# Kernel tuning notes

Measured on AMD Instinct MI355X. Metric: run time of the kernel, lower is better.

The kernel has to match this reference:

```python
import jax, jax.numpy as jnp
import numpy as np

B, S, D, R, N = 4, 2048, 1024, 256, 16

def setup_inputs() -> dict:
    key = jax.random.key(0)
    k1, k2, k3, k4, k5 = jax.random.split(key, 5)
    return {
        "x": jax.random.normal(k1, (B, S, D), dtype=jnp.float32),
        "feature_know": jax.random.normal(k2, (N, D, R), dtype=jnp.float32) * 0.02,
        "restore_know": jax.random.normal(k3, (N, R, D), dtype=jnp.float32) * 0.02,
        "feature_know_w": jax.random.uniform(k4, (B, S, N), dtype=jnp.float32),
        "restore_know_w": jax.random.uniform(k5, (B, S, N), dtype=jnp.float32),
    }

def reference(x, feature_know, restore_know, feature_know_w, restore_know_w):
    # Feature stage: weighted mixture over N knowledge neurons, D -> R.
    # Same math as einsum('bsd,ndr->bsnr') then einsum('bsnr,bsn->bsr'),
    # fused so the [B,S,N,R] intermediate is reduced over N on the fly.
    h = jnp.einsum('bsd,ndr,bsn->bsr', x, feature_know, feature_know_w)
    # Restore stage: R -> D, again a weighted mixture over N neurons.
    out = jnp.einsum('bsr,nrd,bsn->bsd', h, restore_know, restore_know_w)
    # Dropout is evaluated deterministically (eval mode): identity.
    return out
```

## Files before the change

### kernel.cpp

```cpp
#include <hip/hip_runtime.h>

typedef unsigned short u16;
typedef unsigned int u32;
typedef __attribute__((ext_vector_type(4))) float f32x4;
typedef __attribute__((ext_vector_type(8))) short bf16x8;
typedef __attribute__((ext_vector_type(4))) unsigned short u16x4;

#define MFMA(a, b, c) __builtin_amdgcn_mfma_f32_16x16x32_bf16((a), (b), (c), 0, 0, 0)

static constexpr int M_TOK = 8192;

__device__ __forceinline__ u16 f2bf(float f) {
  u32 u = __float_as_uint(f);
  return (u16)((u + 0x7FFFu + ((u >> 16) & 1u)) >> 16);
}
__device__ __forceinline__ float bf2f(u16 b) {
  u32 u = ((u32)b) << 16;
  return __uint_as_float(u);
}
__device__ __forceinline__ void gload16(const u16* g, u16* l) {
  __builtin_amdgcn_global_load_lds(
      (const __attribute__((address_space(1))) u32*)(const void*)g,
      (__attribute__((address_space(3))) u32*)(void*)l, 16, 0, 0);
}

#define PH_BAR()                                     \
  do {                                               \
    __builtin_amdgcn_sched_barrier(0);               \
    __builtin_amdgcn_s_barrier();                    \
    asm volatile("s_waitcnt lgkmcnt(0)" ::: "memory"); \
    __builtin_amdgcn_sched_barrier(0);               \
  } while (0)
#define PH_END()                       \
  do {                                 \
    __builtin_amdgcn_sched_barrier(0); \
    __builtin_amdgcn_s_barrier();      \
  } while (0)

__global__ void cast_x_kernel(const float* __restrict__ in, u16* __restrict__ out, int total4) {
  for (int i = blockIdx.x * blockDim.x + threadIdx.x; i < total4; i += gridDim.x * blockDim.x) {
    float4 v = ((const float4*)in)[i];
    u16x4 o;
    o[0] = f2bf(v.x); o[1] = f2bf(v.y); o[2] = f2bf(v.z); o[3] = f2bf(v.w);
    ((u16x4*)out)[i] = o;
  }
}

__global__ void tcast_kernel(const float* __restrict__ in, u16* __restrict__ out, int P, int Q) {
  __shared__ float tile[32][33];
  const int z = blockIdx.z;
  const int q0 = blockIdx.x * 32, p0 = blockIdx.y * 32;
  const float* src = in + (size_t)z * P * Q;
  u16* dst = out + (size_t)z * P * Q;
  const int tx = threadIdx.x & 31, ty = threadIdx.x >> 5;
#pragma unroll
  for (int k = 0; k < 4; ++k)
    tile[ty + k * 8][tx] = src[(size_t)(p0 + ty + k * 8) * Q + q0 + tx];
  __syncthreads();
#pragma unroll
  for (int k = 0; k < 4; ++k)
    dst[(size_t)(q0 + ty + k * 8) * P + p0 + tx] = f2bf(tile[tx][ty + k * 8]);
}

__global__ void combine_h(const u16* __restrict__ T, const float* __restrict__ Wf,
                          u16* __restrict__ h) {
  const int m = blockIdx.x * 4 + (threadIdx.x >> 6);
  const int lane = threadIdx.x & 63;
  const u16* rowp = T + (size_t)m * 4096;
  float h0 = 0.f, h1 = 0.f, h2 = 0.f, h3 = 0.f;
#pragma unroll
  for (int n = 0; n < 16; ++n) {
    u16x4 v = *(const u16x4*)&rowp[n * 256 + lane * 4];
    const float wf = Wf[(size_t)m * 16 + n];
    h0 += wf * bf2f(v[0]); h1 += wf * bf2f(v[1]);
    h2 += wf * bf2f(v[2]); h3 += wf * bf2f(v[3]);
  }
  u16x4 o;
  o[0] = f2bf(h0); o[1] = f2bf(h1); o[2] = f2bf(h2); o[3] = f2bf(h3);
  *(u16x4*)&h[(size_t)m * 256 + lane * 4] = o;
}

template <int NT>
__global__ __launch_bounds__(512, 2) void gemm256(
    const u16* __restrict__ A, const u16* __restrict__ Bm, void* __restrict__ OutV,
    const int N, const int K) {
  constexpr int NITER = NT / 2;
  __shared__ u16 ldsA[2][2][8192];
  __shared__ u16 ldsB[2][2][8192];

  const int tid = threadIdx.x;
  const int lane = tid & 63;
  const int wid = tid >> 6;
  const int wr = wid >> 2, wc = wid & 3;

  {
  }
  const int L = blockIdx.y * gridDim.x + blockIdx.x;
  const int ordered = (L & 7) * 64 + (L >> 3);
  const int cid = ordered >> 5, win = ordered & 31;
  const int bx = (cid & 3) * 4 + (win & 3);
  const int by = (cid >> 2) * 8 + (win >> 2);
  const int m0 = by * 256, bn0 = bx * 256;

  const int arow = lane & 15;
  const int acol = (lane >> 4) * 16;
  const int sw = (arow & 7) << 4;
  const int lo0 = arow * 128 + (acol ^ sw);
  const int lo1 = arow * 128 + ((64 + acol) ^ sw);

  const u16* Abase = A + (size_t)m0 * K;
  const u16* Bbase = Bm + (size_t)bn0 * K;

  f32x4 acc[8][4];
#pragma unroll
  for (int i = 0; i < 8; ++i)
#pragma unroll
    for (int j = 0; j < 4; ++j) acc[i][j] = (f32x4){0.f, 0.f, 0.f, 0.f};

  auto STAGE = [&](int b, int isB, int hf, int kt) {
    const u16* G = isB ? Bbase : Abase;
    u16* L2p = isB ? &ldsB[b][hf][0] : &ldsA[b][hf][0];
#pragma unroll
    for (int j = 0; j < 2; ++j) {
      const int q = j * 8192 + tid * 16;
      const int grow = q >> 7;
      const int gcol = ((q & 127) ^ (((q >> 7) & 7) << 4)) >> 1;
      gload16(G + (size_t)(hf * 128 + grow) * K + kt * 64 + gcol,
              L2p + ((j * 8192 + wid * 1024) >> 1));
    }
  };
  auto LOAD_AV = [&](bf16x8 (&v)[4][2], int b, int mh) {
    const char* p = (const char*)&ldsA[b][0][0] + (wr * 128 + mh * 64) * 128;
#pragma unroll
    for (int mi = 0; mi < 4; ++mi) {
      v[mi][0] = *(const bf16x8*)(p + mi * 2048 + lo0);
      v[mi][1] = *(const bf16x8*)(p + mi * 2048 + lo1);
    }
  };
  auto LOAD_BV = [&](bf16x8 (&v)[2][2], int b, int nq) {
#pragma unroll
    for (int nj = 0; nj < 2; ++nj) {
      const int rb = wc * 64 + (nq * 2 + nj) * 16;
      const char* p = (const char*)&ldsB[b][0][0] + rb * 128;
      v[nj][0] = *(const bf16x8*)(p + lo0);
      v[nj][1] = *(const bf16x8*)(p + lo1);
    }
  };

#define QUAD(AV, BV, MH, NQ)                                                   \
  do {                                                                         \
    _Pragma("unroll") for (int mi = 0; mi < 4; ++mi) {                         \
      _Pragma("unroll") for (int nj = 0; nj < 2; ++nj) {                       \
        acc[(MH)*4 + mi][(NQ)*2 + nj] =                                        \
            MFMA(AV[mi][0], BV[nj][0], acc[(MH)*4 + mi][(NQ)*2 + nj]);         \
        acc[(MH)*4 + mi][(NQ)*2 + nj] =                                        \
            MFMA(AV[mi][1], BV[nj][1], acc[(MH)*4 + mi][(NQ)*2 + nj]);         \
      }                                                                        \
    }                                                                          \
  } while (0)

  bf16x8 av[4][2], avh[4][2], bv0[2][2], bv1[2][2];

  STAGE(0, 0, 0, 0); STAGE(0, 0, 1, 0); STAGE(0, 1, 0, 0); STAGE(0, 1, 1, 0);
  STAGE(1, 1, 0, 1); STAGE(1, 0, 0, 1);
  asm volatile("s_waitcnt vmcnt(4)" ::: "memory");
  __builtin_amdgcn_sched_barrier(0);
  __builtin_amdgcn_s_barrier();

#pragma unroll 1
  for (int i = 0; i < NITER; ++i) {
    const int ta = 2 * i, tb = ta + 1;
    const bool st = (i + 1 < NITER);
    LOAD_AV(av, 0, 0); LOAD_BV(bv0, 0, 0); LOAD_BV(bv1, 0, 1);
    STAGE(1, 0, 1, tb); STAGE(1, 1, 1, tb);
    PH_BAR();
    __builtin_amdgcn_s_setprio(1);
    QUAD(av, bv0, 0, 0); QUAD(av, bv1, 0, 1);
    __builtin_amdgcn_s_setprio(0);
    PH_END();
    LOAD_AV(avh, 0, 1);
    if (st) { STAGE(0, 1, 0, ta + 2); STAGE(0, 0, 0, ta + 2); }
    PH_BAR();
    __builtin_amdgcn_s_setprio(1);
    QUAD(avh, bv0, 1, 0); QUAD(avh, bv1, 1, 1);
    __builtin_amdgcn_s_setprio(0);
    if (st) asm volatile("s_waitcnt vmcnt(4)" ::: "memory");
    else    asm volatile("s_waitcnt vmcnt(0)" ::: "memory");
    PH_END();
    LOAD_AV(av, 1, 0); LOAD_BV(bv0, 1, 0); LOAD_BV(bv1, 1, 1);
    if (st) { STAGE(0, 0, 1, ta + 2); STAGE(0, 1, 1, ta + 2); }
    PH_BAR();
    __builtin_amdgcn_s_setprio(1);
    QUAD(av, bv0, 0, 0); QUAD(av, bv1, 0, 1);
    __builtin_amdgcn_s_setprio(0);
    PH_END();
    LOAD_AV(avh, 1, 1);
    if (st) { STAGE(1, 1, 0, tb + 2); STAGE(1, 0, 0, tb + 2); }
    PH_BAR();
    __builtin_amdgcn_s_setprio(1);
    QUAD(avh, bv0, 1, 0); QUAD(avh, bv1, 1, 1);
    __builtin_amdgcn_s_setprio(0);
    if (st) asm volatile("s_waitcnt vmcnt(4)" ::: "memory");
    PH_END();
  }

#pragma unroll
  for (int MI = 0; MI < 8; ++MI) {
    const int row = m0 + wr * 128 + MI * 16 + (lane >> 4) * 4;
#pragma unroll
    for (int NJ = 0; NJ < 4; ++NJ) {
      const int col = bn0 + wc * 64 + NJ * 16 + (lane & 15);
      u16* p = (u16*)OutV + (size_t)row * N + col;
#pragma unroll
      for (int j = 0; j < 4; ++j) p[(size_t)j * N] = f2bf(acc[MI][NJ][j]);
    }
  }
}
#undef QUAD

__global__ __launch_bounds__(512, 2) void gemm_fold(
    const u16* __restrict__ A,
    const u16* __restrict__ Bn,
    const float* __restrict__ W,
    float* __restrict__ Out) {
  __shared__ u16 ldsB[8][8192];
  __shared__ u16 Wlds[16][264];

  const int tid = threadIdx.x;
  const int lane = tid & 63;
  const int wid = tid >> 6;
  const int kh = wid >> 2;
  const int wrM = (wid >> 1) & 1;
  const int wcN = wid & 1;

  const int L = blockIdx.y * gridDim.x + blockIdx.x;
  const int ordered = (L & 7) * 64 + (L >> 3);
  const int cid = ordered >> 5, win = ordered & 31;
  const int bx = (cid & 3) * 2 + (win & 1);
  const int by = (cid >> 2) * 16 + (win >> 1);
  const int m0 = by * 128, d0 = bx * 128;

  const int arow = lane & 15;
  const int acol = (lane >> 4) * 16;
  const int sw = (arow & 7) << 4;
  const int lo0 = arow * 128 + (acol ^ sw);
  const int lo1 = arow * 128 + ((64 + acol) ^ sw);

  for (int i = tid; i < 128 * 16; i += 512) {
    const int row = i >> 4, n = i & 15;
    Wlds[n][row] = f2bf(W[(size_t)(m0 + row) * 16 + n]);
  }

  auto ASTAGE = [&](int kt) {
    const u16* G = A + (size_t)m0 * 256;
    u16* Lp = &ldsB[kt][0];
#pragma unroll
    for (int j = 0; j < 2; ++j) {
      const int q = j * 8192 + tid * 16;
      const int grow = q >> 7;
      const int gcol = ((q & 127) ^ (((q >> 7) & 7) << 4)) >> 1;
      gload16(G + (size_t)grow * 256 + kt * 64 + gcol, Lp + ((j * 8192 + wid * 1024) >> 1));
    }
  };
  ASTAGE(0); ASTAGE(1); ASTAGE(2); ASTAGE(3);
  __syncthreads();
  bf16x8 avk[4][4];
#pragma unroll
  for (int c2 = 0; c2 < 2; ++c2) {
#pragma unroll
    for (int mi = 0; mi < 4; ++mi) {
      const char* p = (const char*)&ldsB[kh * 2 + c2][0] + (wrM * 64 + mi * 16) * 128;
      avk[c2 * 2 + 0][mi] = *(const bf16x8*)(p + lo0);
      avk[c2 * 2 + 1][mi] = *(const bf16x8*)(p + lo1);
    }
  }
  __syncthreads();

  auto BSTAGE = [&](int ss) {
    const int n = ss >> 1, h = ss & 1, p = ss & 3;
    const u16* G = Bn + ((size_t)n * 1024 + d0) * 256;
#pragma unroll
    for (int t = 0; t < 2; ++t) {
      u16* Lp = &ldsB[2 * p + t][0];
      const int kt = h + 2 * t;
#pragma unroll
      for (int j = 0; j < 2; ++j) {
        const int q = j * 8192 + tid * 16;
        const int grow = q >> 7;
        const int gcol = ((q & 127) ^ (((q >> 7) & 7) << 4)) >> 1;
        gload16(G + (size_t)grow * 256 + kt * 64 + gcol, Lp + ((j * 8192 + wid * 1024) >> 1));
      }
    }
  };

  f32x4 acc_t[4][4], acc_g[4][4];
#pragma unroll
  for (int mi = 0; mi < 4; ++mi)
#pragma unroll
    for (int nj = 0; nj < 4; ++nj) {
      acc_t[mi][nj] = (f32x4){0.f, 0.f, 0.f, 0.f};
      acc_g[mi][nj] = (f32x4){0.f, 0.f, 0.f, 0.f};
    }
  bf16x8 bv[4][2];

  BSTAGE(0); BSTAGE(1); BSTAGE(2);
  asm volatile("s_waitcnt vmcnt(8)" ::: "memory");
  __builtin_amdgcn_sched_barrier(0);
  __builtin_amdgcn_s_barrier();

  auto SSTEP = [&](int ss, int h, bool do_stage, int vmsel) {
    const int p = ss & 3;
    const char* pB = (const char*)&ldsB[2 * p + kh][0];
#pragma unroll
    for (int nj = 0; nj < 4; ++nj) {
      const char* q = pB + (wcN * 64 + nj * 16) * 128;
      bv[nj][0] = *(const bf16x8*)(q + lo0);
      bv[nj][1] = *(const bf16x8*)(q + lo1);
    }
    if (do_stage) BSTAGE(ss + 3);
    PH_BAR();
    __builtin_amdgcn_s_setprio(1);
#pragma unroll
    for (int mi = 0; mi < 4; ++mi)
#pragma unroll
      for (int nj = 0; nj < 4; ++nj) {
        acc_g[mi][nj] = MFMA(avk[2 * h + 0][mi], bv[nj][0], acc_g[mi][nj]);
        acc_g[mi][nj] = MFMA(avk[2 * h + 1][mi], bv[nj][1], acc_g[mi][nj]);
      }
    __builtin_amdgcn_s_setprio(0);
    if (vmsel == 8)      asm volatile("s_waitcnt vmcnt(8)" ::: "memory");
    else if (vmsel == 4) asm volatile("s_waitcnt vmcnt(4)" ::: "memory");
    else if (vmsel == 0) asm volatile("s_waitcnt vmcnt(0)" ::: "memory");
    PH_END();
  };
  auto FOLD = [&](int n) {
#pragma unroll
    for (int mi = 0; mi < 4; ++mi) {
      const int rbase = wrM * 64 + mi * 16 + (lane >> 4) * 4;
      u16x4 wq = *(const u16x4*)&Wlds[n][rbase];
      const float w0 = bf2f(wq[0]), w1 = bf2f(wq[1]), w2 = bf2f(wq[2]), w3 = bf2f(wq[3]);
#pragma unroll
      for (int nj = 0; nj < 4; ++nj) {
        acc_t[mi][nj][0] += w0 * acc_g[mi][nj][0];
        acc_t[mi][nj][1] += w1 * acc_g[mi][nj][1];
        acc_t[mi][nj][2] += w2 * acc_g[mi][nj][2];
        acc_t[mi][nj][3] += w3 * acc_g[mi][nj][3];
        acc_g[mi][nj] = (f32x4){0.f, 0.f, 0.f, 0.f};
      }
    }
  };

#pragma unroll 1
  for (int nn = 0; nn < 14; ++nn) {
    SSTEP(nn * 2 + 0, 0, true, 8);
    SSTEP(nn * 2 + 1, 1, true, 8);
    FOLD(nn);
  }
  SSTEP(28, 0, true, 8);
  SSTEP(29, 1, false, 4);
  FOLD(14);
  SSTEP(30, 0, false, 0);
  SSTEP(31, 1, false, -1);
  FOLD(15);

  __syncthreads();
  float* red = (float*)&ldsB[0][0];
  const int reg = (wrM * 2 + wcN) * 4096;
  if (kh == 1) {
#pragma unroll
    for (int mi = 0; mi < 4; ++mi)
#pragma unroll
      for (int j = 0; j < 4; ++j) {
        const int r = mi * 16 + (lane >> 4) * 4 + j;
#pragma unroll
        for (int nj = 0; nj < 4; ++nj)
          red[reg + r * 64 + nj * 16 + (lane & 15)] = acc_t[mi][nj][j];
      }
  }
  __syncthreads();
  if (kh == 0) {
#pragma unroll
    for (int mi = 0; mi < 4; ++mi) {
      const int rr = mi * 16 + (lane >> 4) * 4;
#pragma unroll
      for (int j = 0; j < 4; ++j) {
        float* orow = Out + (size_t)(m0 + wrM * 64 + rr + j) * 1024 + d0 + wcN * 64 + (lane & 15);
#pragma unroll
        for (int nj = 0; nj < 4; ++nj)
          orow[nj * 16] = acc_t[mi][nj][j] + red[reg + (rr + j) * 64 + nj * 16 + (lane & 15)];
      }
    }
  }
}

extern "C" void kernel_launch(void* const* d_in, const int* in_sizes, int n_in,
                              void* d_out, int out_size, void* d_ws, size_t ws_size,
                              hipStream_t stream) {
  const float* x  = (const float*)d_in[0];
  const float* F  = (const float*)d_in[1];
  const float* Rk = (const float*)d_in[2];
  const float* Wf = (const float*)d_in[3];
  const float* Wr = (const float*)d_in[4];
  float* out = (float*)d_out;

  char* ws = (char*)d_ws;
  u16* X16 = (u16*)(ws);
  u16* B1  = (u16*)(ws + (16u << 20));
  u16* Rt  = (u16*)(ws + (24u << 20));
  u16* T   = (u16*)(ws + (32u << 20));
  u16* h16 = (u16*)(ws);

  cast_x_kernel<<<2048, 256, 0, stream>>>(x, X16, (M_TOK * 1024) / 4);
  tcast_kernel<<<dim3(8, 32, 16), 256, 0, stream>>>(F, B1, 1024, 256);
  tcast_kernel<<<dim3(32, 8, 16), 256, 0, stream>>>(Rk, Rt, 256, 1024);

  gemm256<16><<<dim3(16, 32, 1), 512, 0, stream>>>(X16, B1, T, 4096, 1024);
  combine_h<<<2048, 256, 0, stream>>>(T, Wf, h16);
  gemm_fold<<<dim3(8, 64, 1), 512, 0, stream>>>(h16, Rt, Wr, out);
}
```

Before: 171.0 us.

## Stage GEMM epilogues through swizzled LDS for coalesced vector stores; reorder MFMA k-loop

Both GEMM kernels now write their output tiles into a swizzled LDS buffer first and then store them to global memory with 16-byte vector writes, replacing the scattered 2- and 4-byte per-lane stores. The fold kernel's cross-half reduction also goes through this LDS tile before the coalesced write. The MFMA loops are reordered so the k-slice index is outermost, which spaces out dependent accumulator updates. The cost is extra LDS traffic and barriers in the epilogue, plus reuse of the operand LDS buffers for output staging.

```diff
diff --git a/kernel.cpp b/kernel.cpp
--- a/kernel.cpp
+++ b/kernel.cpp
@@ -85,16 +85,13 @@
     const u16* __restrict__ A, const u16* __restrict__ Bm, void* __restrict__ OutV,
     const int N, const int K) {
   constexpr int NITER = NT / 2;
-  __shared__ u16 ldsA[2][2][8192];
-  __shared__ u16 ldsB[2][2][8192];
+  __shared__ u16 lds[65536];
 
   const int tid = threadIdx.x;
   const int lane = tid & 63;
   const int wid = tid >> 6;
   const int wr = wid >> 2, wc = wid & 3;
 
-  {
-  }
   const int L = blockIdx.y * gridDim.x + blockIdx.x;
   const int ordered = (L & 7) * 64 + (L >> 3);
   const int cid = ordered >> 5, win = ordered & 31;
@@ -119,18 +116,18 @@
 
   auto STAGE = [&](int b, int isB, int hf, int kt) {
     const u16* G = isB ? Bbase : Abase;
-    u16* L2p = isB ? &ldsB[b][hf][0] : &ldsA[b][hf][0];
+    u16* Lp = &lds[isB * 32768 + (b * 2 + hf) * 8192];
 #pragma unroll
     for (int j = 0; j < 2; ++j) {
       const int q = j * 8192 + tid * 16;
       const int grow = q >> 7;
       const int gcol = ((q & 127) ^ (((q >> 7) & 7) << 4)) >> 1;
       gload16(G + (size_t)(hf * 128 + grow) * K + kt * 64 + gcol,
-              L2p + ((j * 8192 + wid * 1024) >> 1));
+              Lp + ((j * 8192 + wid * 1024) >> 1));
     }
   };
   auto LOAD_AV = [&](bf16x8 (&v)[4][2], int b, int mh) {
-    const char* p = (const char*)&ldsA[b][0][0] + (wr * 128 + mh * 64) * 128;
+    const char* p = (const char*)lds + b * 32768 + (wr * 128 + mh * 64) * 128;
 #pragma unroll
     for (int mi = 0; mi < 4; ++mi) {
       v[mi][0] = *(const bf16x8*)(p + mi * 2048 + lo0);
@@ -141,20 +138,20 @@
 #pragma unroll
     for (int nj = 0; nj < 2; ++nj) {
       const int rb = wc * 64 + (nq * 2 + nj) * 16;
-      const char* p = (const char*)&ldsB[b][0][0] + rb * 128;
+      const char* p = (const char*)lds + 65536 + b * 32768 + rb * 128;
       v[nj][0] = *(const bf16x8*)(p + lo0);
       v[nj][1] = *(const bf16x8*)(p + lo1);
     }
   };
 
-#define QUAD(AV, BV, MH, NQ)                                                   \
+#define QUAD2(AV, BV0, BV1, MH)                                                \
   do {                                                                         \
-    _Pragma("unroll") for (int mi = 0; mi < 4; ++mi) {                         \
-      _Pragma("unroll") for (int nj = 0; nj < 2; ++nj) {                       \
-        acc[(MH)*4 + mi][(NQ)*2 + nj] =                                        \
-            MFMA(AV[mi][0], BV[nj][0], acc[(MH)*4 + mi][(NQ)*2 + nj]);         \
-        acc[(MH)*4 + mi][(NQ)*2 + nj] =                                        \
-            MFMA(AV[mi][1], BV[nj][1], acc[(MH)*4 + mi][(NQ)*2 + nj]);         \
+    _Pragma("unroll") for (int ks = 0; ks < 2; ++ks) {                         \
+      _Pragma("unroll") for (int mi = 0; mi < 4; ++mi) {                       \
+        _Pragma("unroll") for (int nj = 0; nj < 2; ++nj) {                     \
+          acc[(MH)*4 + mi][nj] = MFMA(AV[mi][ks], BV0[nj][ks], acc[(MH)*4 + mi][nj]); \
+          acc[(MH)*4 + mi][2 + nj] = MFMA(AV[mi][ks], BV1[nj][ks], acc[(MH)*4 + mi][2 + nj]); \
+        }                                                                      \
       }                                                                        \
     }                                                                          \
   } while (0)
@@ -175,14 +172,14 @@
     STAGE(1, 0, 1, tb); STAGE(1, 1, 1, tb);
     PH_BAR();
     __builtin_amdgcn_s_setprio(1);
-    QUAD(av, bv0, 0, 0); QUAD(av, bv1, 0, 1);
+    QUAD2(av, bv0, bv1, 0);
     __builtin_amdgcn_s_setprio(0);
     PH_END();
     LOAD_AV(avh, 0, 1);
     if (st) { STAGE(0, 1, 0, ta + 2); STAGE(0, 0, 0, ta + 2); }
     PH_BAR();
     __builtin_amdgcn_s_setprio(1);
-    QUAD(avh, bv0, 1, 0); QUAD(avh, bv1, 1, 1);
+    QUAD2(avh, bv0, bv1, 1);
     __builtin_amdgcn_s_setprio(0);
     if (st) asm volatile("s_waitcnt vmcnt(4)" ::: "memory");
     else    asm volatile("s_waitcnt vmcnt(0)" ::: "memory");
@@ -191,14 +188,14 @@
     if (st) { STAGE(0, 0, 1, ta + 2); STAGE(0, 1, 1, ta + 2); }
     PH_BAR();
     __builtin_amdgcn_s_setprio(1);
-    QUAD(av, bv0, 0, 0); QUAD(av, bv1, 0, 1);
+    QUAD2(av, bv0, bv1, 0);
     __builtin_amdgcn_s_setprio(0);
     PH_END();
     LOAD_AV(avh, 1, 1);
     if (st) { STAGE(1, 1, 0, tb + 2); STAGE(1, 0, 0, tb + 2); }
     PH_BAR();
     __builtin_amdgcn_s_setprio(1);
-    QUAD(avh, bv0, 1, 0); QUAD(avh, bv1, 1, 1);
+    QUAD2(avh, bv0, bv1, 1);
     __builtin_amdgcn_s_setprio(0);
     if (st) asm volatile("s_waitcnt vmcnt(4)" ::: "memory");
     PH_END();
@@ -206,17 +203,27 @@
 
 #pragma unroll
   for (int MI = 0; MI < 8; ++MI) {
-    const int row = m0 + wr * 128 + MI * 16 + (lane >> 4) * 4;
+    const int r0 = wr * 128 + MI * 16 + (lane >> 4) * 4;
 #pragma unroll
     for (int NJ = 0; NJ < 4; ++NJ) {
-      const int col = bn0 + wc * 64 + NJ * 16 + (lane & 15);
-      u16* p = (u16*)OutV + (size_t)row * N + col;
-#pragma unroll
-      for (int j = 0; j < 4; ++j) p[(size_t)j * N] = f2bf(acc[MI][NJ][j]);
-    }
-  }
-}
-#undef QUAD
+      const int c = wc * 64 + NJ * 16 + (lane & 15);
+#pragma unroll
+      for (int j = 0; j < 4; ++j) {
+        const int rr = r0 + j;
+        *(u16*)((char*)lds + ((rr * 512 + c * 2) ^ ((rr & 7) << 4))) = f2bf(acc[MI][NJ][j]);
+      }
+    }
+  }
+  __syncthreads();
+#pragma unroll
+  for (int i = 0; i < 16; ++i) {
+    const int rr = wid * 32 + i * 2 + (lane >> 5);
+    const int unit = lane & 31;
+    bf16x8 v = *(const bf16x8*)((const char*)lds + ((rr * 512 + unit * 16) ^ ((rr & 7) << 4)));
+    *(bf16x8*)((u16*)OutV + (size_t)(m0 + rr) * N + bn0 + unit * 8) = v;
+  }
+}
+#undef QUAD2
 
 __global__ __launch_bounds__(512, 2) void gemm_fold(
     const u16* __restrict__ A,
@@ -321,12 +328,12 @@
     PH_BAR();
     __builtin_amdgcn_s_setprio(1);
 #pragma unroll
-    for (int mi = 0; mi < 4; ++mi)
-#pragma unroll
-      for (int nj = 0; nj < 4; ++nj) {
-        acc_g[mi][nj] = MFMA(avk[2 * h + 0][mi], bv[nj][0], acc_g[mi][nj]);
-        acc_g[mi][nj] = MFMA(avk[2 * h + 1][mi], bv[nj][1], acc_g[mi][nj]);
-      }
+    for (int ks = 0; ks < 2; ++ks)
+#pragma unroll
+      for (int mi = 0; mi < 4; ++mi)
+#pragma unroll
+        for (int nj = 0; nj < 4; ++nj)
+          acc_g[mi][nj] = MFMA(avk[2 * h + ks][mi], bv[nj][ks], acc_g[mi][nj]);
     __builtin_amdgcn_s_setprio(0);
     if (vmsel == 8)      asm volatile("s_waitcnt vmcnt(8)" ::: "memory");
     else if (vmsel == 4) asm volatile("s_waitcnt vmcnt(4)" ::: "memory");
@@ -364,32 +371,40 @@
   FOLD(15);
 
   __syncthreads();
-  float* red = (float*)&ldsB[0][0];
-  const int reg = (wrM * 2 + wcN) * 4096;
+  char* red = (char*)&ldsB[0][0];
+  auto rb = [&](int r, int c) { return (r * 512 + c * 4) ^ ((r & 7) << 4); };
   if (kh == 1) {
 #pragma unroll
     for (int mi = 0; mi < 4; ++mi)
 #pragma unroll
       for (int j = 0; j < 4; ++j) {
-        const int r = mi * 16 + (lane >> 4) * 4 + j;
+        const int r = wrM * 64 + mi * 16 + (lane >> 4) * 4 + j;
 #pragma unroll
         for (int nj = 0; nj < 4; ++nj)
-          red[reg + r * 64 + nj * 16 + (lane & 15)] = acc_t[mi][nj][j];
+          *(float*)(red + rb(r, wcN * 64 + nj * 16 + (lane & 15))) = acc_t[mi][nj][j];
       }
   }
   __syncthreads();
   if (kh == 0) {
 #pragma unroll
-    for (int mi = 0; mi < 4; ++mi) {
-      const int rr = mi * 16 + (lane >> 4) * 4;
+    for (int mi = 0; mi < 4; ++mi)
 #pragma unroll
       for (int j = 0; j < 4; ++j) {
-        float* orow = Out + (size_t)(m0 + wrM * 64 + rr + j) * 1024 + d0 + wcN * 64 + (lane & 15);
-#pragma unroll
-        for (int nj = 0; nj < 4; ++nj)
-          orow[nj * 16] = acc_t[mi][nj][j] + red[reg + (rr + j) * 64 + nj * 16 + (lane & 15)];
+        const int r = wrM * 64 + mi * 16 + (lane >> 4) * 4 + j;
+#pragma unroll
+        for (int nj = 0; nj < 4; ++nj) {
+          float* p = (float*)(red + rb(r, wcN * 64 + nj * 16 + (lane & 15)));
+          *p += acc_t[mi][nj][j];
+        }
       }
-    }
+  }
+  __syncthreads();
+#pragma unroll
+  for (int i = 0; i < 8; ++i) {
+    const int r = wid * 16 + i * 2 + (lane >> 5);
+    const int unit = lane & 31;
+    f32x4 v = *(const f32x4*)(red + ((r * 512 + unit * 16) ^ ((r & 7) << 4)));
+    *(f32x4*)(Out + (size_t)(m0 + r) * 1024 + d0 + unit * 4) = v;
   }
 }
 
```

After: 174.8 us. +2.2%, slower.
